# Optimization experiments

Measured on AMD Instinct MI355X. Metric: run time of the kernel, lower is better.

## Reference

```python
import jax, jax.numpy as jnp
import numpy as np

N_MELS = 128
N_STATE = 1024
N_HEAD = 8
N_LAYER = 6
STRIDE = 2
HEAD_DIM = N_STATE // N_HEAD  # 128; must equal N_MELS for the rope buffer to broadcast
B = 8
T = 4096


def setup_inputs():
    key = jax.random.key(0)
    ks = iter(jax.random.split(key, 40))
    def rn(shape, s=0.02):
        return jax.random.normal(next(ks), shape, dtype=jnp.float32) * s
    L, D, F = N_LAYER, N_STATE, 4 * N_STATE
    inp = {}
    inp['x'] = jax.random.normal(next(ks), (B, N_MELS, T), dtype=jnp.float32)
    inp['x_len'] = jax.random.randint(next(ks), (B,), T // 2, T + 1)
    inp['conv1_w'] = rn((D, N_MELS, 3))
    inp['conv1_b'] = jnp.zeros((D,), jnp.float32)
    inp['conv2_w'] = rn((D, D, 3))
    inp['conv2_b'] = jnp.zeros((D,), jnp.float32)
    inp['attn_ln_w'] = jnp.ones((L, D), jnp.float32)
    inp['attn_ln_b'] = jnp.zeros((L, D), jnp.float32)
    inp['q_w'] = rn((L, D, D)); inp['q_b'] = jnp.zeros((L, D), jnp.float32)
    inp['k_w'] = rn((L, D, D))
    inp['v_w'] = rn((L, D, D)); inp['v_b'] = jnp.zeros((L, D), jnp.float32)
    inp['out_w'] = rn((L, D, D)); inp['out_b'] = jnp.zeros((L, D), jnp.float32)
    inp['mlp_ln_w'] = jnp.ones((L, D), jnp.float32)
    inp['mlp_ln_b'] = jnp.zeros((L, D), jnp.float32)
    inp['mlp1_w'] = rn((L, F, D)); inp['mlp1_b'] = jnp.zeros((L, F), jnp.float32)
    inp['mlp2_w'] = rn((L, D, F)); inp['mlp2_b'] = jnp.zeros((L, D), jnp.float32)
    return inp


def _ln(x, w, b, eps=1e-5):
    x = x.astype(jnp.float32)
    m = jnp.mean(x, -1, keepdims=True)
    v = jnp.mean((x - m) ** 2, -1, keepdims=True)
    return (x - m) * jax.lax.rsqrt(v + eps) * w + b


def _conv1d(x, w, b, stride):
    # x: [B, Cin, T]; w: [Cout, Cin, K] (torch OIH layout); pad=1
    y = jax.lax.conv_general_dilated(x, w, (stride,), [(1, 1)],
                                     dimension_numbers=('NCH', 'OIH', 'NCH'))
    return y + b[None, :, None]


def reference(x, x_len, conv1_w, conv1_b, conv2_w, conv2_b,
              attn_ln_w, attn_ln_b, q_w, q_b, k_w, v_w, v_b, out_w, out_b,
              mlp_ln_w, mlp_ln_b, mlp1_w, mlp1_b, mlp2_w, mlp2_b):
    Tin = x.shape[-1]
    h = jax.nn.gelu(_conv1d(x, conv1_w, conv1_b, STRIDE), approximate=False)
    h = jax.nn.gelu(_conv1d(h, conv2_w, conv2_b, 2), approximate=False)
    h = jnp.transpose(h, (0, 2, 1))  # [B, S, D]
    S = h.shape[1]

    # non-pad mask over original mel frames, subsampled like the conv stack
    mask = jnp.arange(Tin)[None, :] < x_len[:, None]
    mask = mask[:, (Tin + 1) % 2::2]
    if STRIDE == 2:
        Tm = mask.shape[-1]
        mask = mask[:, (Tm + 1) % 2::2]
    bias = ((1.0 - mask.astype(jnp.float32)) * -1.0e10)[:, None, None, :]  # [B,1,1,S]

    # rotary embedding table (freqs_cis as cos/sin), dim == HEAD_DIM == N_MELS
    half = HEAD_DIM // 2
    freqs = 1.0 / (10000.0 ** (jnp.arange(0, HEAD_DIM, 2, dtype=jnp.float32) / HEAD_DIM))
    ang = jnp.arange(S, dtype=jnp.float32)[:, None] * freqs[None, :]  # [S, half]
    cos = jnp.cos(ang)[None, :, None, :]
    sin = jnp.sin(ang)[None, :, None, :]
    scale = HEAD_DIM ** (-0.25)

    def rot(t):  # t: [B,S,H,HEAD_DIM], interleaved (re, im) pairs
        tr = t.reshape(t.shape[0], t.shape[1], N_HEAD, half, 2)
        re, im = tr[..., 0], tr[..., 1]
        return jnp.stack([re * cos - im * sin, re * sin + im * cos], -1)\
                  .reshape(t.shape[0], t.shape[1], N_HEAD, HEAD_DIM)

    def block(carry, p):
        aw, ab, qw, qb, kw, vw, vb, ow, ob, mw, mb, w1, b1, w2, b2 = p
        y = _ln(carry, aw, ab)
        q = y @ qw.T + qb
        k = y @ kw.T          # key has no bias
        v = y @ vw.T + vb
        Bb, Ss = q.shape[0], q.shape[1]
        q = rot(q.reshape(Bb, Ss, N_HEAD, HEAD_DIM)) * scale
        k = rot(k.reshape(Bb, Ss, N_HEAD, HEAD_DIM)) * scale
        v = v.reshape(Bb, Ss, N_HEAD, HEAD_DIM)
        qk = jnp.einsum('bqhd,bkhd->bhqk', q, k) + bias
        w = jax.nn.softmax(qk.astype(jnp.float32), axis=-1)
        o = jnp.einsum('bhqk,bkhd->bqhd', w, v).reshape(Bb, Ss, N_STATE)
        carry = carry + o @ ow.T + ob
        y = _ln(carry, mw, mb)
        y = jax.nn.gelu(y @ w1.T + b1, approximate=False) @ w2.T + b2
        return carry + y, None

    params = (attn_ln_w, attn_ln_b, q_w, q_b, k_w, v_w, v_b, out_w, out_b,
              mlp_ln_w, mlp_ln_b, mlp1_w, mlp1_b, mlp2_w, mlp2_b)
    h, _ = jax.lax.scan(block, h, params)

    y_len = (x_len + 1) // 2
    if STRIDE == 2:
        y_len = (y_len + 1) // 2
    return h, y_len
```

## Files before the change

kernel.cpp:

```cpp
#include <hip/hip_runtime.h>
#include <hip/hip_bf16.h>
#include <cstdint>
#include <cstddef>


typedef __bf16 bf16_t;
typedef __bf16 bf16x8 __attribute__((ext_vector_type(8)));
typedef __bf16 bf16x4 __attribute__((ext_vector_type(4)));
typedef float  floatx4 __attribute__((ext_vector_type(4)));

#define NB   8
#define NS   1024
#define ND   1024
#define NT   4096
#define NT1  2048

#define MFMA16(a, b, c) __builtin_amdgcn_mfma_f32_16x16x32_bf16(a, b, c, 0, 0, 0)

#define SBAR() do { __builtin_amdgcn_sched_barrier(0); \
                    __builtin_amdgcn_s_barrier();      \
                    __builtin_amdgcn_sched_barrier(0); } while (0)

__device__ __forceinline__ float gelu_f(float x) {
  const float t = 1.5957691216057308f * (x + 0.044715f * x * x * x);
  return x / (1.0f + __expf(-t));
}

__device__ __forceinline__ void gload16(const void* g, void* l) {
  __builtin_amdgcn_global_load_lds(
      (__attribute__((address_space(1))) void*)(const_cast<void*>(g)),
      (__attribute__((address_space(3))) void*)l, 16, 0, 0);
}

enum { EPI_BF16 = 0, EPI_GELU_BF16 = 2, EPI_GELU_F32 = 3, EPI_RES_F32 = 4, EPI_QKV = 5 };

__device__ __forceinline__ void xcd_remap(int& bx, int& by) {
  const int gx = gridDim.x, gy = gridDim.y;
  const int id  = bx + by * gx;
  const int xcd = id & 7;
  const int r   = id >> 3;
  const int cby = (gx * gy) >> 7;
  const int ncx = gx >> 4;
  const int cx  = xcd % ncx, cy = xcd / ncx;
  bx = cx * 16 + (r & 15);
  by = cy * cby + (r >> 4);
}

#define COMPUTE2(BUF, H) { \
    const char* rAd = rA + (BUF) * 16384 + (H) * 8192; \
    const char* rBd = rB + (BUF) * 16384 + (H) * 8192; \
    const bf16x8 a0 = *(const bf16x8*)(rAd +    0); \
    const bf16x8 a1 = *(const bf16x8*)(rAd + 1024); \
    const bf16x8 a2 = *(const bf16x8*)(rAd + 2048); \
    const bf16x8 a3 = *(const bf16x8*)(rAd + 3072); \
    const bf16x8 b0 = *(const bf16x8*)(rBd +    0); \
    const bf16x8 b1 = *(const bf16x8*)(rBd + 1024); \
    acc[0][0] = MFMA16(a0, b0, acc[0][0]); acc[0][1] = MFMA16(a0, b1, acc[0][1]); \
    acc[1][0] = MFMA16(a1, b0, acc[1][0]); acc[1][1] = MFMA16(a1, b1, acc[1][1]); \
    acc[2][0] = MFMA16(a2, b0, acc[2][0]); acc[2][1] = MFMA16(a2, b1, acc[2][1]); \
    acc[3][0] = MFMA16(a3, b0, acc[3][0]); acc[3][1] = MFMA16(a3, b1, acc[3][1]); \
  }

#define KSTEP(BUF, SNEXT_OK) do { \
    if (SNEXT_OK) { \
      gload16(aP,      dA + ((BUF) ^ 1) * 8192);        \
      gload16(aP + 32, dA + ((BUF) ^ 1) * 8192 + 4096); \
    } \
    COMPUTE2(BUF, 0); \
    if (SNEXT_OK) { \
      gload16(bP,      dB + ((BUF) ^ 1) * 8192);        \
      gload16(bP + 32, dB + ((BUF) ^ 1) * 8192 + 4096); \
      aP += 64; bP += 64; \
    } \
    COMPUTE2(BUF, 1); \
    asm volatile("s_waitcnt vmcnt(0)" ::: "memory"); \
    SBAR(); \
  } while (0)

template<int EPI>
__global__ __launch_bounds__(512, 4)
void gemm_bt(const bf16_t* __restrict__ A, long lda,
             const bf16_t* __restrict__ Bm, long ldb,
             void* Cv, long ldc,
             const float* __restrict__ bias, const float* res,
             int K, int swz,
             bf16_t* out2, bf16_t* out3, const float* __restrict__ bias2,
             const float2* __restrict__ rtab)
{
  __shared__ bf16_t sA[2][8192];
  __shared__ bf16_t sB[2][8192];
  const int tid  = threadIdx.x;
  const int wid  = tid >> 6;
  const int lane = tid & 63;
  const int lo = lane & 15, g = lane >> 4;
  const int wr = wid >> 2, wc = wid & 3;

  int bx = blockIdx.x, by = blockIdx.y;
  if (swz) xcd_remap(bx, by);
  const int m0 = bx * 128, n0 = by * 128;
  const int NTK = K >> 6;

  const int lrow = lane >> 2;
  const int lcol = 8 * ((lane & 3) ^ ((lane >> 3) & 3));
  const int rslot = 16 * (g ^ ((lo >> 1) & 3));

  const bf16_t* aP = A  + (long)(m0 + wid * 16 + lrow) * lda + lcol;
  const bf16_t* bP = Bm + (long)(n0 + wid * 16 + lrow) * ldb + lcol;
  bf16_t* const dA = &sA[0][wid * 512];
  bf16_t* const dB = &sB[0][wid * 512];
  const char* const rA = (const char*)&sA[0][0] + (wr * 64 + lo) * 64 + rslot;
  const char* const rB = (const char*)&sB[0][0] + (wc * 32 + lo) * 64 + rslot;

  floatx4 acc[4][2] = {};

  gload16(aP,      dA);         gload16(aP + 32, dA + 4096);
  gload16(bP,      dB);         gload16(bP + 32, dB + 4096);
  aP += 64; bP += 64;
  asm volatile("s_waitcnt vmcnt(0)" ::: "memory");
  SBAR();

#pragma unroll 1
  for (int s = 0; s < NTK; s += 2) {
    KSTEP(0, (s + 1 < NTK));
    KSTEP(1, (s + 2 < NTK));
  }

  if constexpr (EPI == EPI_QKV) {
    const int sect = n0 >> 10;
#pragma unroll
    for (int ni = 0; ni < 2; ++ni) {
      const int col = n0 + wc * 32 + ni * 16 + lo;
      const int c10 = col & 1023;
      float bvs = 0.0f;
      if (sect == 0) bvs = bias[c10];
      else if (sect == 2) bvs = bias2[c10];
#pragma unroll
      for (int mi = 0; mi < 4; ++mi) {
#pragma unroll
        for (int r = 0; r < 4; ++r) {
          const int row = m0 + wr * 64 + mi * 16 + g * 4 + r;
          const int sr = row & 1023;
          float val = acc[mi][ni][r] + bvs;
          if (sect < 2) {
            const float2 t = rtab[(sr << 6) + ((col & 127) >> 1)];
            const float p = __shfl_xor(val, 1);
            val = val * t.x + p * ((col & 1) ? t.y : -t.y);
            bf16_t* dst = sect ? out2 : (bf16_t*)Cv;
            dst[(long)row * 1024 + c10] = (bf16_t)val;
          } else {
            out3[((long)(row >> 10) << 20) + ((long)(col - 2048) << 10) + sr] = (bf16_t)val;
          }
        }
      }
    }
    return;
  }

#pragma unroll
  for (int ni = 0; ni < 2; ++ni) {
    const int col = n0 + wc * 32 + ni * 16 + lo;
    const float bvs = bias ? bias[col] : 0.0f;
#pragma unroll
    for (int mi = 0; mi < 4; ++mi) {
#pragma unroll
      for (int r = 0; r < 4; ++r) {
        const int row = m0 + wr * 64 + mi * 16 + g * 4 + r;
        float v = acc[mi][ni][r] + bvs;
        if constexpr (EPI == EPI_BF16) {
          ((bf16_t*)Cv)[(long)row * ldc + col] = (bf16_t)v;
        } else if constexpr (EPI == EPI_GELU_BF16) {
          ((bf16_t*)Cv)[(long)row * ldc + col] = (bf16_t)gelu_f(v);
        } else if constexpr (EPI == EPI_GELU_F32) {
          ((float*)Cv)[(long)row * ldc + col] = gelu_f(v);
        } else {
          const long idx = (long)row * ldc + col;
          ((float*)Cv)[idx] = res[idx] + v;
        }
      }
    }
  }
}

__global__ __launch_bounds__(256, 4)
void flash_kernel(const bf16_t* __restrict__ q, const bf16_t* __restrict__ k,
                  const bf16_t* __restrict__ vt, bf16_t* __restrict__ o,
                  const int* __restrict__ xlen)
{
  __shared__ bf16_t sK[2][4096];
  __shared__ bf16_t sV[2][4096];
  __shared__ bf16_t sP[4][512];
  const int tid = threadIdx.x, w = tid >> 6, lane = tid & 63;
  const int lo = lane & 15, g = lane >> 4;
  const int hid = blockIdx.x + (blockIdx.y << 4);
  const int h   = hid & 7;
  const int qx  = (hid >> 3) & 15;
  const int b   = hid >> 7;
  const int q0 = qx * 64 + w * 16;
  const int nv  = xlen[b] >> 2;
  const int nkt = (nv + 31) >> 5;
  const long base = (long)b * 1048576 + (long)h * 128;
  const bf16_t* Qp = q + base;
  const bf16_t* Kp = k + base;
  const bf16_t* Vp = vt + (long)b * 1048576 + ((long)h << 17);

  auto stageKV = [&](int kt, int buf) {
    const int kv0 = kt << 5;
#pragma unroll
    for (int jj = 0; jj < 2; ++jj) {
      const int seg = (w << 1) + jj;
      {
        const int row = (seg << 2) + (lane >> 4);
        const int col = ((lane & 15) << 3) ^ ((row & 7) << 3);
        gload16(Kp + (long)(kv0 + row) * 1024 + col, &sK[buf][seg * 512]);
      }
      {
        const int row = (seg << 4) + (lane >> 2);
        const int col = ((lane & 3) << 3) ^ ((row & 3) << 3);
        gload16(Vp + (long)row * 1024 + kv0 + col, &sV[buf][seg * 512]);
      }
    }
  };

  bf16x8 qf[4];
#pragma unroll
  for (int ks = 0; ks < 4; ++ks)
    qf[ks] = *reinterpret_cast<const bf16x8*>(
        Qp + (long)(q0 + lo) * 1024 + ks * 32 + g * 8);

  floatx4 of[8] = {};
  float m[4], l[4];
#pragma unroll
  for (int r = 0; r < 4; ++r) { m[r] = -1e30f; l[r] = 0.0f; }

  const char* kbase = (const char*)&sK[0][0];
  const char* vbase = (const char*)&sV[0][0];
  char* pbase = (char*)&sP[w][0];
  const int swzK = (lo & 7) << 4;
  const int swzV = (lo & 3) << 4;

  stageKV(0, 0);
  __syncthreads();
  int cur = 0;
#pragma unroll 1
  for (int kt = 0; kt < nkt; ++kt) {
    const int kv0 = kt << 5;
    if (kt + 1 < nkt) stageKV(kt + 1, cur ^ 1);

    floatx4 s[2] = {};
    __builtin_amdgcn_s_setprio(1);
#pragma unroll
    for (int ni = 0; ni < 2; ++ni) {
#pragma unroll
      for (int ks = 0; ks < 4; ++ks) {
        const bf16x8 bv = *reinterpret_cast<const bf16x8*>(
            kbase + cur * 8192 + (ni * 16 + lo) * 256 + ((ks * 64 + (g << 4)) ^ swzK));
        s[ni] = MFMA16(qf[ks], bv, s[ni]);
      }
    }
    __builtin_amdgcn_s_setprio(0);

    float pmv[4];
#pragma unroll
    for (int r = 0; r < 4; ++r) {
      float pm = -1e30f;
#pragma unroll
      for (int ni = 0; ni < 2; ++ni) {
        float val = s[ni][r];
        if (kv0 + ni * 16 + lo >= nv) val = -1e30f;
        pm = fmaxf(pm, val);
      }
      pm = fmaxf(pm, __shfl_xor(pm, 1)); pm = fmaxf(pm, __shfl_xor(pm, 2));
      pm = fmaxf(pm, __shfl_xor(pm, 4)); pm = fmaxf(pm, __shfl_xor(pm, 8));
      pmv[r] = pm;
    }
    const bool skip = __all((pmv[0] <= m[0] + 8.0f) & (pmv[1] <= m[1] + 8.0f) &
                            (pmv[2] <= m[2] + 8.0f) & (pmv[3] <= m[3] + 8.0f));

#pragma unroll
    for (int r = 0; r < 4; ++r) {
      float mn = m[r];
      if (!skip) {
        mn = fmaxf(m[r], pmv[r]);
        const float sc = __expf(m[r] - mn);
        l[r] *= sc;
#pragma unroll
        for (int nd = 0; nd < 8; ++nd) of[nd][r] *= sc;
        m[r] = mn;
      }
      const int qrow = g * 4 + r;
      const int sw = (qrow & 3) << 4;
      float ss = 0.0f;
#pragma unroll
      for (int ni = 0; ni < 2; ++ni) {
        float val = s[ni][r];
        if (kv0 + ni * 16 + lo >= nv) val = -1e30f;
        const float p = __expf(val - mn);
        ss += p;
        *(bf16_t*)(pbase + qrow * 64 + (((ni << 5) + (lo << 1)) ^ sw)) = (bf16_t)p;
      }
      ss += __shfl_xor(ss, 1); ss += __shfl_xor(ss, 2);
      ss += __shfl_xor(ss, 4); ss += __shfl_xor(ss, 8);
      l[r] += ss;
    }

    asm volatile("s_waitcnt lgkmcnt(0)" ::: "memory");
    __builtin_amdgcn_sched_barrier(0);

    __builtin_amdgcn_s_setprio(1);
    {
      const bf16x8 av = *reinterpret_cast<const bf16x8*>(
          pbase + lo * 64 + ((g << 4) ^ swzV));
#pragma unroll
      for (int nd = 0; nd < 8; ++nd) {
        const bf16x8 bv = *reinterpret_cast<const bf16x8*>(
            vbase + cur * 8192 + (nd * 16 + lo) * 64 + ((g << 4) ^ swzV));
        of[nd] = MFMA16(av, bv, of[nd]);
      }
    }
    __builtin_amdgcn_s_setprio(0);
    __syncthreads();
    cur ^= 1;
  }

#pragma unroll
  for (int r = 0; r < 4; ++r) {
    const float inv = 1.0f / l[r];
    const long rb = base + (long)(q0 + g * 4 + r) * 1024;
#pragma unroll
    for (int nd = 0; nd < 8; ++nd)
      o[rb + nd * 16 + lo] = (bf16_t)(of[nd][r] * inv);
  }
}

__global__ __launch_bounds__(256)
void ln_kernel(const float* __restrict__ x, bf16_t* __restrict__ y,
               const float* __restrict__ w, const float* __restrict__ b)
{
  const long row = blockIdx.x;
  const float4 v = reinterpret_cast<const float4*>(x + row * ND)[threadIdx.x];
  float s  = v.x + v.y + v.z + v.w;
  float ss = v.x * v.x + v.y * v.y + v.z * v.z + v.w * v.w;
#pragma unroll
  for (int off = 32; off; off >>= 1) { s += __shfl_down(s, off); ss += __shfl_down(ss, off); }
  __shared__ float sh[8];
  if ((threadIdx.x & 63) == 0) { sh[threadIdx.x >> 6] = s; sh[4 + (threadIdx.x >> 6)] = ss; }
  __syncthreads();
  const float tot  = sh[0] + sh[1] + sh[2] + sh[3];
  const float tot2 = sh[4] + sh[5] + sh[6] + sh[7];
  const float mean = tot * (1.0f / ND);
  const float var  = tot2 * (1.0f / ND) - mean * mean;
  const float rstd = rsqrtf(var + 1e-5f);
  const int i0 = threadIdx.x * 4;
  const float vv[4] = {v.x, v.y, v.z, v.w};
  bf16x4 o;
#pragma unroll
  for (int j = 0; j < 4; ++j)
    o[j] = (bf16_t)((vv[j] - mean) * rstd * w[i0 + j] + b[i0 + j]);
  reinterpret_cast<bf16x4*>(y + row * ND)[threadIdx.x] = o;
}

__global__ __launch_bounds__(256)
void rtab_kernel(float2* __restrict__ tab)
{
  const int idx = blockIdx.x * 256 + threadIdx.x;
  const int s = idx >> 6, i = idx & 63;
  const float freq = __expf((float)i * -0.14391156831212787f);
  float sn, cs;
  sincosf((float)s * freq, &sn, &cs);
  const float sc = 0.29730177875068026f;
  tab[idx] = make_float2(cs * sc, sn * sc);
}

__global__ __launch_bounds__(256)
void im2col1_kernel(const float* __restrict__ x, bf16_t* __restrict__ a)
{
  const long idx = (long)blockIdx.x * 256 + threadIdx.x;
  if (idx >= (long)NB * NT1 * 384) return;
  const int  k = (int)(idx % 384);
  const long m = idx / 384;
  const int i = k / 3, kk = k - 3 * i;
  const int t = (int)(m & (NT1 - 1));
  const int b = (int)(m >> 11);
  const int tt = 2 * t + kk - 1;
  float v = 0.0f;
  if (tt >= 0 && tt < NT) v = x[((long)b * 128 + i) * NT + tt];
  a[idx] = (bf16_t)v;
}

__global__ __launch_bounds__(256)
void im2col2_kernel(const bf16_t* __restrict__ h1, bf16_t* __restrict__ a)
{
  const long idx = (long)blockIdx.x * 256 + threadIdx.x;
  if (idx >= (long)NB * NS * 3072) return;
  const int  k = (int)(idx % 3072);
  const long m = idx / 3072;
  const int i = k / 3, kk = k - 3 * i;
  const int t = (int)(m & (NS - 1));
  const int b = (int)(m >> 10);
  const int tt = 2 * t + kk - 1;
  bf16_t v = (bf16_t)0.0f;
  if (tt >= 0 && tt < NT1) v = h1[((long)b * NT1 + tt) * ND + i];
  a[idx] = v;
}

__global__ void ylen_kernel(const int* __restrict__ xlen, float* __restrict__ ylen)
{
  const int b = threadIdx.x;
  if (b < NB) {
    const int y1 = (xlen[b] + 1) >> 1;
    ylen[b] = (float)((y1 + 1) >> 1);
  }
}

__global__ __launch_bounds__(256)
void cvt_kernel(const float* __restrict__ in, bf16_t* __restrict__ out, long n)
{
  const long i = ((long)blockIdx.x * 256 + threadIdx.x) * 4;
  if (i >= n) return;
  const float4 v = *reinterpret_cast<const float4*>(in + i);
  bf16x4 o;
  o[0] = (bf16_t)v.x; o[1] = (bf16_t)v.y; o[2] = (bf16_t)v.z; o[3] = (bf16_t)v.w;
  *reinterpret_cast<bf16x4*>(out + i) = o;
}

__global__ __launch_bounds__(256)
void cvt_layer_kernel(const float* __restrict__ qw, const float* __restrict__ kw,
                      const float* __restrict__ vw, const float* __restrict__ ow,
                      const float* __restrict__ w1, const float* __restrict__ w2,
                      bf16_t* __restrict__ wqkv, bf16_t* __restrict__ wo,
                      bf16_t* __restrict__ w1b, bf16_t* __restrict__ w2b)
{
  const long i = ((long)blockIdx.x * 256 + threadIdx.x) * 4;
  const float* src; bf16_t* dst;
  if (i < 3145728) {
    dst = wqkv + i;
    if (i < 1048576)      { src = qw + i; }
    else if (i < 2097152) { src = kw + (i - 1048576); }
    else                  { src = vw + (i - 2097152); }
  } else if (i < 4194304) { src = ow + (i - 3145728); dst = wo  + (i - 3145728); }
  else if (i < 8388608)   { src = w1 + (i - 4194304); dst = w1b + (i - 4194304); }
  else                    { src = w2 + (i - 8388608); dst = w2b + (i - 8388608); }
  const float4 v = *reinterpret_cast<const float4*>(src);
  bf16x4 o;
  o[0] = (bf16_t)v.x; o[1] = (bf16_t)v.y; o[2] = (bf16_t)v.z; o[3] = (bf16_t)v.w;
  *reinterpret_cast<bf16x4*>(dst) = o;
}

extern "C" void kernel_launch(void* const* d_in, const int* in_sizes, int n_in,
                              void* d_out, int out_size, void* d_ws, size_t ws_size,
                              hipStream_t stream)
{
  const float* x         = (const float*)d_in[0];
  const int*   x_len     = (const int*)  d_in[1];
  const float* conv1_w   = (const float*)d_in[2];
  const float* conv1_b   = (const float*)d_in[3];
  const float* conv2_w   = (const float*)d_in[4];
  const float* conv2_b   = (const float*)d_in[5];
  const float* attn_ln_w = (const float*)d_in[6];
  const float* attn_ln_b = (const float*)d_in[7];
  const float* q_w   = (const float*)d_in[8];
  const float* q_b   = (const float*)d_in[9];
  const float* k_w   = (const float*)d_in[10];
  const float* v_w   = (const float*)d_in[11];
  const float* v_b   = (const float*)d_in[12];
  const float* out_w = (const float*)d_in[13];
  const float* out_b = (const float*)d_in[14];
  const float* mlp_ln_w = (const float*)d_in[15];
  const float* mlp_ln_b = (const float*)d_in[16];
  const float* mlp1_w = (const float*)d_in[17];
  const float* mlp1_b = (const float*)d_in[18];
  const float* mlp2_w = (const float*)d_in[19];
  const float* mlp2_b = (const float*)d_in[20];
  float* outp = (float*)d_out;
  (void)in_sizes; (void)n_in; (void)out_size;

  const long MB = 1024L * 1024;
  char* ws = (char*)d_ws;
  size_t off = 0;
  auto alloc = [&](size_t bytes) -> char* {
    char* p = ws + off;
    off += (bytes + 255) & ~(size_t)255;
    return p;
  };
  bf16_t* ybuf  = (bf16_t*)alloc(16 * MB);
  bf16_t* qbuf  = (bf16_t*)alloc(16 * MB);
  char*   R     = alloc(64 * MB);
  char*   wA    = alloc(25 * MB);
  const size_t required = off;

  bf16_t* a1  = ybuf;
  bf16_t* h1  = qbuf;
  bf16_t* a2  = (bf16_t*)(R + 16 * MB);
  bf16_t* c2w = (bf16_t*)wA;
  bf16_t* c1w = (bf16_t*)(wA + 8 * MB);
  float2* rtab = (float2*)(wA + 6 * MB);
  bf16_t* wqkv = (bf16_t*)wA;
  bf16_t* wo   = (bf16_t*)(wA + 6 * MB + 512 * 1024);
  bf16_t* w1b  = (bf16_t*)(wA + 9 * MB);
  bf16_t* w2b  = (bf16_t*)(wA + 17 * MB);
  bf16_t* kbuf = (bf16_t*)R;
  bf16_t* vt   = (bf16_t*)(R + 16 * MB);
  bf16_t* hid  = (bf16_t*)R;

  if (required > ws_size) {
    ylen_kernel<<<dim3(1), 64, 0, stream>>>(x_len, outp + 8L * 1024 * 1024);
    return;
  }

  auto cvt = [&](const float* in, bf16_t* o, long n) {
    cvt_kernel<<<dim3((unsigned)(n / 1024)), 256, 0, stream>>>(in, o, n);
  };

  rtab_kernel<<<dim3(256), 256, 0, stream>>>(rtab);

  cvt(conv1_w, c1w, 1024L * 384);
  cvt(conv2_w, c2w, 1024L * 3072);
  im2col1_kernel<<<dim3((unsigned)((16384L * 384) / 256)), 256, 0, stream>>>(x, a1);
  gemm_bt<EPI_GELU_BF16><<<dim3(128, 8), 512, 0, stream>>>(
      a1, 384, c1w, 384, h1, 1024, conv1_b, nullptr, 384, 1,
      nullptr, nullptr, nullptr, nullptr);
  im2col2_kernel<<<dim3((unsigned)((8192L * 3072) / 256)), 256, 0, stream>>>(h1, a2);
  gemm_bt<EPI_GELU_F32><<<dim3(64, 8), 512, 0, stream>>>(
      a2, 3072, c2w, 3072, outp , 1024, conv2_b, nullptr, 3072, 1,
      nullptr, nullptr, nullptr, nullptr);

  float* carry = outp;

  for (int l = 0; l < 6; ++l) {
    cvt_layer_kernel<<<dim3(12288), 256, 0, stream>>>(
        q_w + (long)l * 1048576, k_w + (long)l * 1048576, v_w + (long)l * 1048576,
        out_w + (long)l * 1048576, mlp1_w + (long)l * 4194304, mlp2_w + (long)l * 4194304,
        wqkv, wo, w1b, w2b);

    ln_kernel<<<dim3(8192), 256, 0, stream>>>(carry, ybuf, attn_ln_w + l * 1024, attn_ln_b + l * 1024);

    gemm_bt<EPI_QKV><<<dim3(64, 24), 512, 0, stream>>>(
        ybuf, 1024, wqkv, 1024, qbuf, 1024,
        q_b + l * 1024, nullptr, 1024, 1, kbuf, vt, v_b + l * 1024, rtab);

    flash_kernel<<<dim3(16, 64), 256, 0, stream>>>(qbuf, kbuf, vt, qbuf, x_len);

    gemm_bt<EPI_RES_F32><<<dim3(64, 8), 512, 0, stream>>>(
        qbuf, 1024, wo, 1024, carry, 1024,
        out_b + l * 1024, carry, 1024, 1, nullptr, nullptr, nullptr, nullptr);

    ln_kernel<<<dim3(8192), 256, 0, stream>>>(carry, ybuf, mlp_ln_w + l * 1024, mlp_ln_b + l * 1024);

    gemm_bt<EPI_GELU_BF16><<<dim3(64, 32), 512, 0, stream>>>(
        ybuf, 1024, w1b, 1024, hid, 4096,
        mlp1_b + (long)l * 4096, nullptr, 1024, 1, nullptr, nullptr, nullptr, nullptr);
    gemm_bt<EPI_RES_F32><<<dim3(64, 8), 512, 0, stream>>>(
        hid, 4096, w2b, 4096, carry, 1024,
        mlp2_b + l * 1024, carry, 4096, 1, nullptr, nullptr, nullptr, nullptr);
  }

  ylen_kernel<<<dim3(1), 64, 0, stream>>>(x_len, outp + 8L * 1024 * 1024);
}
```

Baseline: 2.602 ms.

## Split-K the MLP down-projection GEMM with atomic accumulation into residual

Replaces the MLP2 GEMM (K=4096, 512 blocks) with a new split-K kernel that divides K into two halves, launching 1024 blocks whose partial products are atomically added into the fp32 residual carry, with the bias added only by the first split. This is meant to raise occupancy and parallelism for the long-K GEMM, which had few output tiles. The cost is fp32 atomic traffic on the carry buffer and a nondeterministic summation order. It also uses a simpler single-stage double-buffer loop with a 128x128 tile.

New measurement: 2.840 ms. 1.09x slower.

```diff
diff --git a/kernel.cpp b/kernel.cpp
--- a/kernel.cpp
+++ b/kernel.cpp
@@ -176,6 +176,91 @@
           const long idx = (long)row * ldc + col;
           ((float*)Cv)[idx] = res[idx] + v;
         }
+      }
+    }
+  }
+}
+
+#define COMPUTE1(BUF) { \
+    const char* rAd = rA + (BUF) * 8192; \
+    const char* rBd = rB + (BUF) * 8192; \
+    const bf16x8 a0 = *(const bf16x8*)(rAd +    0); \
+    const bf16x8 a1 = *(const bf16x8*)(rAd + 1024); \
+    const bf16x8 a2 = *(const bf16x8*)(rAd + 2048); \
+    const bf16x8 a3 = *(const bf16x8*)(rAd + 3072); \
+    const bf16x8 b0 = *(const bf16x8*)(rBd +    0); \
+    const bf16x8 b1 = *(const bf16x8*)(rBd + 1024); \
+    acc[0][0] = MFMA16(a0, b0, acc[0][0]); acc[0][1] = MFMA16(a0, b1, acc[0][1]); \
+    acc[1][0] = MFMA16(a1, b0, acc[1][0]); acc[1][1] = MFMA16(a1, b1, acc[1][1]); \
+    acc[2][0] = MFMA16(a2, b0, acc[2][0]); acc[2][1] = MFMA16(a2, b1, acc[2][1]); \
+    acc[3][0] = MFMA16(a3, b0, acc[3][0]); acc[3][1] = MFMA16(a3, b1, acc[3][1]); \
+  }
+
+#define KSTEP1(BUF, OK) do { \
+    if (OK) { \
+      gload16(aP, dA + ((BUF) ^ 1) * 4096); \
+      gload16(bP, dB + ((BUF) ^ 1) * 4096); \
+      aP += 32; bP += 32; \
+    } \
+    COMPUTE1(BUF); \
+    asm volatile("s_waitcnt vmcnt(0)" ::: "memory"); \
+    SBAR(); \
+  } while (0)
+
+__global__ __launch_bounds__(512, 8)
+void gemm_bt2(const bf16_t* __restrict__ A, long lda,
+              const bf16_t* __restrict__ Bm, long ldb,
+              float* __restrict__ carry, long ldc,
+              const float* __restrict__ bias, int HK)
+{
+  __shared__ bf16_t sA[2][4096];
+  __shared__ bf16_t sB[2][4096];
+  const int tid  = threadIdx.x;
+  const int wid  = tid >> 6;
+  const int lane = tid & 63;
+  const int lo = lane & 15, g = lane >> 4;
+  const int wr = wid >> 2, wc = wid & 3;
+
+  int bx = blockIdx.x, by = blockIdx.y;
+  xcd_remap(bx, by);
+  const int kh = by >> 3;
+  const int m0 = bx * 128, n0 = (by & 7) * 128;
+  const int NTK = HK >> 5;
+
+  const int lrow = lane >> 2;
+  const int lcol = 8 * ((lane & 3) ^ ((lane >> 3) & 3));
+  const int rslot = 16 * (g ^ ((lo >> 1) & 3));
+
+  const bf16_t* aP = A  + (long)(m0 + wid * 16 + lrow) * lda + kh * HK + lcol;
+  const bf16_t* bP = Bm + (long)(n0 + wid * 16 + lrow) * ldb + kh * HK + lcol;
+  bf16_t* const dA = &sA[0][wid * 512];
+  bf16_t* const dB = &sB[0][wid * 512];
+  const char* const rA = (const char*)&sA[0][0] + (wr * 64 + lo) * 64 + rslot;
+  const char* const rB = (const char*)&sB[0][0] + (wc * 32 + lo) * 64 + rslot;
+
+  floatx4 acc[4][2] = {};
+
+  gload16(aP, dA); gload16(bP, dB);
+  aP += 32; bP += 32;
+  asm volatile("s_waitcnt vmcnt(0)" ::: "memory");
+  SBAR();
+
+#pragma unroll 1
+  for (int s = 0; s < NTK; s += 2) {
+    KSTEP1(0, (s + 1 < NTK));
+    KSTEP1(1, (s + 2 < NTK));
+  }
+
+#pragma unroll
+  for (int ni = 0; ni < 2; ++ni) {
+    const int col = n0 + wc * 32 + ni * 16 + lo;
+    const float bvs = (kh == 0) ? bias[col] : 0.0f;
+#pragma unroll
+    for (int mi = 0; mi < 4; ++mi) {
+#pragma unroll
+      for (int r = 0; r < 4; ++r) {
+        const int row = m0 + wr * 64 + mi * 16 + g * 4 + r;
+        atomicAdd(&carry[(long)row * ldc + col], acc[mi][ni][r] + bvs);
       }
     }
   }
@@ -549,9 +634,9 @@
     gemm_bt<EPI_GELU_BF16><<<dim3(64, 32), 512, 0, stream>>>(
         ybuf, 1024, w1b, 1024, hid, 4096,
         mlp1_b + (long)l * 4096, nullptr, 1024, 1, nullptr, nullptr, nullptr, nullptr);
-    gemm_bt<EPI_RES_F32><<<dim3(64, 8), 512, 0, stream>>>(
-        hid, 4096, w2b, 4096, carry, 1024,
-        mlp2_b + l * 1024, carry, 4096, 1, nullptr, nullptr, nullptr, nullptr);
+
+    gemm_bt2<<<dim3(64, 16), 512, 0, stream>>>(
+        hid, 4096, w2b, 4096, carry, 1024, mlp2_b + l * 1024, 2048);
   }
 
   ylen_kernel<<<dim3(1), 64, 0, stream>>>(x_len, outp + 8L * 1024 * 1024);
```

## Add 256x128-tile triple-buffered GEMM kernel for MLP1 with fused GELU

Applied to the files above, without the earlier changes.

Adds a dedicated GEMM kernel for the first MLP projection. It uses a larger 256x128 output tile per block, with 64x64 per wave, a three-stage LDS pipeline and swizzled shared-memory reads. The larger tile raises arithmetic intensity and cuts global and LDS traffic per MFMA. In exchange it uses more registers and LDS per block, and the grid shrinks to 1024 blocks, which can lower occupancy.

New measurement: 2.586 ms (median of 2 runs). About the same (-0.6%).

```diff
diff --git a/kernel.cpp b/kernel.cpp
--- a/kernel.cpp
+++ b/kernel.cpp
@@ -176,6 +176,88 @@
           const long idx = (long)row * ldc + col;
           ((float*)Cv)[idx] = res[idx] + v;
         }
+      }
+    }
+  }
+}
+
+__global__ __launch_bounds__(512, 4)
+void gemm_w(const bf16_t* __restrict__ A, long lda,
+            const bf16_t* __restrict__ Bm, long ldb,
+            bf16_t* __restrict__ C, long ldc,
+            const float* __restrict__ bias, int K)
+{
+  __shared__ bf16_t sA[3][8192];
+  __shared__ bf16_t sB[3][4096];
+  const int tid  = threadIdx.x;
+  const int wid  = tid >> 6;
+  const int lane = tid & 63;
+  const int lo = lane & 15, g = lane >> 4;
+  const int wr = wid >> 1, wc = wid & 1;
+
+  int bx = blockIdx.x, by = blockIdx.y;
+  xcd_remap(bx, by);
+  const int m0 = bx * 256, n0 = by * 128;
+  const int NTK = K >> 5;
+
+  const int lrow = lane >> 2;
+  const int lcol = 8 * ((lane & 3) ^ ((lane >> 3) & 3));
+  const int rslot = 16 * (g ^ ((lo >> 1) & 3));
+
+  const bf16_t* a0P = A  + (long)(m0 + (wid * 2)     * 16 + lrow) * lda + lcol;
+  const bf16_t* a1P = A  + (long)(m0 + (wid * 2 + 1) * 16 + lrow) * lda + lcol;
+  const bf16_t* bP  = Bm + (long)(n0 + wid * 16 + lrow) * ldb + lcol;
+  bf16_t* const dA0 = &sA[0][(wid * 2)     * 512];
+  bf16_t* const dA1 = &sA[0][(wid * 2 + 1) * 512];
+  bf16_t* const dB  = &sB[0][wid * 512];
+  const char* const rA = (const char*)&sA[0][0] + (wr * 64 + lo) * 64 + rslot;
+  const char* const rB = (const char*)&sB[0][0] + (wc * 64 + lo) * 64 + rslot;
+
+  floatx4 acc[4][4] = {};
+
+  auto stage = [&](int t) {
+    const int buf = t % 3;
+    gload16(a0P, dA0 + buf * 8192);
+    gload16(a1P, dA1 + buf * 8192);
+    gload16(bP,  dB  + buf * 4096);
+    a0P += 32; a1P += 32; bP += 32;
+  };
+
+  stage(0); stage(1);
+  asm volatile("s_waitcnt vmcnt(3)" ::: "memory");
+  SBAR();
+
+#pragma unroll 1
+  for (int s = 0; s < NTK; ++s) {
+    if (s + 2 < NTK) stage(s + 2);
+    const int buf = s % 3;
+    const char* rAd = rA + buf * 16384;
+    const char* rBd = rB + buf * 8192;
+    bf16x8 av[4], bv[4];
+#pragma unroll
+    for (int i = 0; i < 4; ++i) av[i] = *(const bf16x8*)(rAd + i * 1024);
+#pragma unroll
+    for (int i = 0; i < 4; ++i) bv[i] = *(const bf16x8*)(rBd + i * 1024);
+#pragma unroll
+    for (int mi = 0; mi < 4; ++mi)
+#pragma unroll
+      for (int ni = 0; ni < 4; ++ni)
+        acc[mi][ni] = MFMA16(av[mi], bv[ni], acc[mi][ni]);
+    if (s + 2 < NTK) { asm volatile("s_waitcnt vmcnt(3)" ::: "memory"); }
+    else             { asm volatile("s_waitcnt vmcnt(0)" ::: "memory"); }
+    SBAR();
+  }
+
+#pragma unroll
+  for (int ni = 0; ni < 4; ++ni) {
+    const int col = n0 + wc * 64 + ni * 16 + lo;
+    const float bvs = bias[col];
+#pragma unroll
+    for (int mi = 0; mi < 4; ++mi) {
+#pragma unroll
+      for (int r = 0; r < 4; ++r) {
+        const int row = m0 + wr * 64 + mi * 16 + g * 4 + r;
+        C[(long)row * ldc + col] = (bf16_t)gelu_f(acc[mi][ni][r] + bvs);
       }
     }
   }
@@ -546,9 +628,9 @@
 
     ln_kernel<<<dim3(8192), 256, 0, stream>>>(carry, ybuf, mlp_ln_w + l * 1024, mlp_ln_b + l * 1024);
 
-    gemm_bt<EPI_GELU_BF16><<<dim3(64, 32), 512, 0, stream>>>(
-        ybuf, 1024, w1b, 1024, hid, 4096,
-        mlp1_b + (long)l * 4096, nullptr, 1024, 1, nullptr, nullptr, nullptr, nullptr);
+    gemm_w<<<dim3(32, 32), 512, 0, stream>>>(
+        ybuf, 1024, w1b, 1024, hid, 4096, mlp1_b + (long)l * 4096, 1024);
+
     gemm_bt<EPI_RES_F32><<<dim3(64, 8), 512, 0, stream>>>(
         hid, 4096, w2b, 4096, carry, 1024,
         mlp2_b + l * 1024, carry, 4096, 1, nullptr, nullptr, nullptr, nullptr);
```

## Add 256x256-tile 8-wave GEMM with interleaved LDS pipeline for MLP1

Applied to the files above, without the earlier changes.

Introduces a new gemm8 kernel using 256x256 output tiles, 8 waves, double-buffered LDS filled with direct global-to-LDS loads, and a hand-scheduled ping-pong of LDS reads, prefetches and MFMA quadrants with barriers and priority hints. It replaces the previous 128-wide-tile GEMM for the MLP up-projection with fused GELU epilogue. The larger tile raises arithmetic intensity and cuts global traffic per FLOP, but uses more registers (128 accumulators per thread) and launches fewer blocks (512), so occupancy and tail effects are at risk.

Measured after the change: 2.587 ms. About the same (-0.6%).

```diff
diff --git a/kernel.cpp b/kernel.cpp
--- a/kernel.cpp
+++ b/kernel.cpp
@@ -19,6 +19,9 @@
 
 #define SBAR() do { __builtin_amdgcn_sched_barrier(0); \
                     __builtin_amdgcn_s_barrier();      \
+                    __builtin_amdgcn_sched_barrier(0); } while (0)
+
+#define LGK0() do { asm volatile("s_waitcnt lgkmcnt(0)" ::: "memory"); \
                     __builtin_amdgcn_sched_barrier(0); } while (0)
 
 __device__ __forceinline__ float gelu_f(float x) {
@@ -176,6 +179,152 @@
           const long idx = (long)row * ldc + col;
           ((float*)Cv)[idx] = res[idx] + v;
         }
+      }
+    }
+  }
+}
+
+#define RDA8(DST, BUF, MI0) { \
+    const char* p0_ = rA0 + (BUF) * 32768 + (MI0) * 2048; \
+    const char* p1_ = rA1 + (BUF) * 32768 + (MI0) * 2048; \
+    DST[0][0] = *(const bf16x8*)(p0_);         DST[0][1] = *(const bf16x8*)(p1_); \
+    DST[1][0] = *(const bf16x8*)(p0_ + 2048);  DST[1][1] = *(const bf16x8*)(p1_ + 2048); \
+    DST[2][0] = *(const bf16x8*)(p0_ + 4096);  DST[2][1] = *(const bf16x8*)(p1_ + 4096); \
+    DST[3][0] = *(const bf16x8*)(p0_ + 6144);  DST[3][1] = *(const bf16x8*)(p1_ + 6144); }
+
+#define RDB8(DST, BUF, NI0) { \
+    const char* p0_ = rB0 + (BUF) * 32768 + (NI0) * 2048; \
+    const char* p1_ = rB1 + (BUF) * 32768 + (NI0) * 2048; \
+    DST[0][0] = *(const bf16x8*)(p0_);         DST[0][1] = *(const bf16x8*)(p1_); \
+    DST[1][0] = *(const bf16x8*)(p0_ + 2048);  DST[1][1] = *(const bf16x8*)(p1_ + 2048); }
+
+#define MMQ(M0, N0, AV, BV) { \
+    acc[(M0)+0][(N0)+0] = MFMA16(AV[0][0], BV[0][0], acc[(M0)+0][(N0)+0]); \
+    acc[(M0)+0][(N0)+0] = MFMA16(AV[0][1], BV[0][1], acc[(M0)+0][(N0)+0]); \
+    acc[(M0)+0][(N0)+1] = MFMA16(AV[0][0], BV[1][0], acc[(M0)+0][(N0)+1]); \
+    acc[(M0)+0][(N0)+1] = MFMA16(AV[0][1], BV[1][1], acc[(M0)+0][(N0)+1]); \
+    acc[(M0)+1][(N0)+0] = MFMA16(AV[1][0], BV[0][0], acc[(M0)+1][(N0)+0]); \
+    acc[(M0)+1][(N0)+0] = MFMA16(AV[1][1], BV[0][1], acc[(M0)+1][(N0)+0]); \
+    acc[(M0)+1][(N0)+1] = MFMA16(AV[1][0], BV[1][0], acc[(M0)+1][(N0)+1]); \
+    acc[(M0)+1][(N0)+1] = MFMA16(AV[1][1], BV[1][1], acc[(M0)+1][(N0)+1]); \
+    acc[(M0)+2][(N0)+0] = MFMA16(AV[2][0], BV[0][0], acc[(M0)+2][(N0)+0]); \
+    acc[(M0)+2][(N0)+0] = MFMA16(AV[2][1], BV[0][1], acc[(M0)+2][(N0)+0]); \
+    acc[(M0)+2][(N0)+1] = MFMA16(AV[2][0], BV[1][0], acc[(M0)+2][(N0)+1]); \
+    acc[(M0)+2][(N0)+1] = MFMA16(AV[2][1], BV[1][1], acc[(M0)+2][(N0)+1]); \
+    acc[(M0)+3][(N0)+0] = MFMA16(AV[3][0], BV[0][0], acc[(M0)+3][(N0)+0]); \
+    acc[(M0)+3][(N0)+0] = MFMA16(AV[3][1], BV[0][1], acc[(M0)+3][(N0)+0]); \
+    acc[(M0)+3][(N0)+1] = MFMA16(AV[3][0], BV[1][0], acc[(M0)+3][(N0)+1]); \
+    acc[(M0)+3][(N0)+1] = MFMA16(AV[3][1], BV[1][1], acc[(M0)+3][(N0)+1]); }
+
+#define STG_A8(T, H) if ((T) < NTK) { \
+    const bf16_t* s_ = aP + (long)(T) * 64 + (long)(H) * 128 * lda; \
+    gload16(s_,            dA + (((T) & 1) * 2 + (H)) * 8192); \
+    gload16(s_ + 64 * lda, dA + (((T) & 1) * 2 + (H)) * 8192 + 4096); }
+
+#define STG_B8(T, H) if ((T) < NTK) { \
+    const bf16_t* s_ = bP + (long)(T) * 64 + (long)(H) * 128 * ldb; \
+    gload16(s_,            dB + (((T) & 1) * 2 + (H)) * 8192); \
+    gload16(s_ + 64 * ldb, dB + (((T) & 1) * 2 + (H)) * 8192 + 4096); }
+
+__global__ __launch_bounds__(512, 2)
+void gemm8(const bf16_t* __restrict__ A, long lda,
+           const bf16_t* __restrict__ Bm, long ldb,
+           bf16_t* __restrict__ C, long ldc,
+           const float* __restrict__ bias, int K)
+{
+  __shared__ bf16_t sA[2][2][8192];
+  __shared__ bf16_t sB[2][2][8192];
+  const int tid = threadIdx.x, wid = tid >> 6, lane = tid & 63;
+  const int lo = lane & 15, g = lane >> 4;
+  const int wr = wid >> 2, wc = wid & 3;
+
+  int bx = blockIdx.x, by = blockIdx.y;
+  xcd_remap(bx, by);
+  const int m0 = bx * 256, n0 = by * 256;
+  const int NTK = K >> 6;
+
+  const int trow = tid >> 3;
+  const int tcol = (((tid & 7) ^ ((tid >> 3) & 7)) << 3);
+
+  const bf16_t* aP = A  + (long)(m0 + trow) * lda + tcol;
+  const bf16_t* bP = Bm + (long)(n0 + trow) * ldb + tcol;
+  bf16_t* const dA = &sA[0][0][0] + wid * 512;
+  bf16_t* const dB = &sB[0][0][0] + wid * 512;
+
+  const char* const rA0 = (const char*)&sA[0][0][0] + wr * 16384
+                        + lo * 128 + ((g ^ (lo & 7)) << 4);
+  const char* const rA1 = (const char*)&sA[0][0][0] + wr * 16384
+                        + lo * 128 + (((g + 4) ^ (lo & 7)) << 4);
+  const char* const rB0 = (const char*)&sB[0][0][0] + (wc >> 1) * 16384
+                        + (wc & 1) * 8192 + lo * 128 + ((g ^ (lo & 7)) << 4);
+  const char* const rB1 = (const char*)&sB[0][0][0] + (wc >> 1) * 16384
+                        + (wc & 1) * 8192 + lo * 128 + (((g + 4) ^ (lo & 7)) << 4);
+
+  floatx4 acc[8][4] = {};
+  bf16x8 a[4][2], b01[2][2], b23[2][2];
+
+  STG_A8(0, 0); STG_A8(0, 1);
+  STG_B8(0, 0); STG_B8(0, 1);
+  STG_B8(1, 0); STG_B8(1, 1);
+  asm volatile("s_waitcnt vmcnt(4)" ::: "memory");
+  SBAR();
+
+#pragma unroll 1
+  for (int s = 0; s < NTK; s += 2) {
+    RDA8(a, 0, 0); RDB8(b01, 0, 0);
+    STG_A8(s + 1, 0);
+    SBAR(); LGK0();
+    __builtin_amdgcn_s_setprio(1); MMQ(0, 0, a, b01); __builtin_amdgcn_s_setprio(0);
+    SBAR();
+    RDB8(b23, 0, 2);
+    STG_A8(s + 1, 1);
+    SBAR(); LGK0();
+    __builtin_amdgcn_s_setprio(1); MMQ(0, 2, a, b23); __builtin_amdgcn_s_setprio(0);
+    SBAR();
+    RDA8(a, 0, 4);
+    STG_B8(s + 2, 0);
+    SBAR(); LGK0();
+    __builtin_amdgcn_s_setprio(1); MMQ(4, 2, a, b23); __builtin_amdgcn_s_setprio(0);
+    SBAR();
+    STG_B8(s + 2, 1);
+    SBAR(); LGK0();
+    __builtin_amdgcn_s_setprio(1); MMQ(4, 0, a, b01); __builtin_amdgcn_s_setprio(0);
+    if (s + 2 < NTK) { asm volatile("s_waitcnt vmcnt(4)" ::: "memory"); }
+    else             { asm volatile("s_waitcnt vmcnt(0)" ::: "memory"); }
+    SBAR();
+    RDA8(a, 1, 0); RDB8(b01, 1, 0);
+    STG_A8(s + 2, 0);
+    SBAR(); LGK0();
+    __builtin_amdgcn_s_setprio(1); MMQ(0, 0, a, b01); __builtin_amdgcn_s_setprio(0);
+    SBAR();
+    RDB8(b23, 1, 2);
+    STG_A8(s + 2, 1);
+    SBAR(); LGK0();
+    __builtin_amdgcn_s_setprio(1); MMQ(0, 2, a, b23); __builtin_amdgcn_s_setprio(0);
+    SBAR();
+    RDA8(a, 1, 4);
+    STG_B8(s + 3, 0);
+    SBAR(); LGK0();
+    __builtin_amdgcn_s_setprio(1); MMQ(4, 2, a, b23); __builtin_amdgcn_s_setprio(0);
+    SBAR();
+    STG_B8(s + 3, 1);
+    SBAR(); LGK0();
+    __builtin_amdgcn_s_setprio(1); MMQ(4, 0, a, b01); __builtin_amdgcn_s_setprio(0);
+    if (s + 3 < NTK) { asm volatile("s_waitcnt vmcnt(4)" ::: "memory"); }
+    else             { asm volatile("s_waitcnt vmcnt(0)" ::: "memory"); }
+    SBAR();
+  }
+
+#pragma unroll
+  for (int ni = 0; ni < 4; ++ni) {
+    const int col = n0 + wc * 64 + ni * 16 + lo;
+    const float bvs = bias[col];
+#pragma unroll
+    for (int mi = 0; mi < 8; ++mi) {
+#pragma unroll
+      for (int r = 0; r < 4; ++r) {
+        const int row = m0 + wr * 128 + mi * 16 + g * 4 + r;
+        C[(long)row * ldc + col] = (bf16_t)gelu_f(acc[mi][ni][r] + bvs);
       }
     }
   }
@@ -546,9 +695,9 @@
 
     ln_kernel<<<dim3(8192), 256, 0, stream>>>(carry, ybuf, mlp_ln_w + l * 1024, mlp_ln_b + l * 1024);
 
-    gemm_bt<EPI_GELU_BF16><<<dim3(64, 32), 512, 0, stream>>>(
-        ybuf, 1024, w1b, 1024, hid, 4096,
-        mlp1_b + (long)l * 4096, nullptr, 1024, 1, nullptr, nullptr, nullptr, nullptr);
+    gemm8<<<dim3(32, 16), 512, 0, stream>>>(
+        ybuf, 1024, w1b, 1024, hid, 4096, mlp1_b + (long)l * 4096, 1024);
+
     gemm_bt<EPI_RES_F32><<<dim3(64, 8), 512, 0, stream>>>(
         hid, 4096, w2b, 4096, carry, 1024,
         mlp2_b + l * 1024, carry, 4096, 1, nullptr, nullptr, nullptr, nullptr);
```
